# Performance work log

Measured on AMD Instinct MI355X. Metric: run time of the kernel, lower is better.

Reference implementation:

```python
import jax, jax.numpy as jnp
import numpy as np

N = 96                       # max_num_nodes == input_dim
LATENT = 256
OUT_DIM = N * (N + 1) // 2   # 4656
MPM_ITERS = 50


def setup_inputs() -> dict:
    key = jax.random.key(0)
    ks = jax.random.split(key, 8)
    s = 0.05
    return {
        "input_features": jax.random.normal(ks[0], (1, N, N), jnp.float32),
        "adj": jax.random.uniform(ks[1], (1, N, N), jnp.float32),
        "eps": jax.random.normal(ks[2], (1, LATENT), jnp.float32),
        "We11": jax.random.normal(ks[3], (N * N, LATENT), jnp.float32) * s,
        "be11": jnp.zeros((LATENT,), jnp.float32),
        "We12": jax.random.normal(ks[4], (N * N, LATENT), jnp.float32) * s,
        "be12": jnp.zeros((LATENT,), jnp.float32),
        "Wd1": jax.random.normal(ks[5], (LATENT, LATENT), jnp.float32) * s,
        "bd1": jnp.zeros((LATENT,), jnp.float32),
        "Wd2": jax.random.normal(ks[6], (LATENT, OUT_DIM), jnp.float32) * s,
        "bd2": jnp.zeros((OUT_DIM,), jnp.float32),
    }


def _bce(inp, tgt):
    # torch F.binary_cross_entropy(input=inp, target=tgt) with log clamp -100
    li = jnp.clip(jnp.log(inp), -100.0)
    l1 = jnp.clip(jnp.log1p(-inp), -100.0)
    return -jnp.mean(tgt * li + (1.0 - tgt) * l1)


def reference(input_features, adj, eps, We11, be11, We12, be12, Wd1, bd1, Wd2, bd2):
    # ---- MLP_VAE_plain ----
    h = input_features.reshape(-1, N * N)              # [1, N*N]
    z_mu = h @ We11 + be11
    z_ls = h @ We12 + be12
    z = eps * jnp.exp(0.5 * z_ls) + z_mu
    y = jax.nn.relu(z @ Wd1 + bd1) @ Wd2 + bd2         # [1, OUT_DIM]
    out = jax.nn.sigmoid(y)

    # ---- recover recon adjacency from triu vector (detached in original) ----
    iu, ju = jnp.triu_indices(N)
    up = jnp.zeros((N, N), jnp.float32).at[iu, ju].set(out[0])
    adj_rec = up + up.T - jnp.diag(jnp.diag(up))

    adj0 = adj[0]
    feat = jnp.sum(adj0, axis=1)                       # degree features
    feat_r = jnp.sum(adj_rec, axis=1)

    # ---- edge similarity tensor S[i,j,a,b] (vectorized O(N^4)) ----
    d = jnp.diag(adj0)
    dr = jnp.diag(adj_rec)
    A = adj0 * d[:, None] * d[None, :]                 # adj[i,j]*adj[i,i]*adj[j,j]
    B = adj_rec * dr[:, None] * dr[None, :]
    off = 1.0 - jnp.eye(N, dtype=jnp.float32)
    S = (A * off)[:, :, None, None] * (B * off)[None, None, :, :]  # i!=j, a!=b
    sim = 1.0 / (jnp.abs(feat[:, None] - feat_r[None, :]) + 1.0)   # deg_feature_similarity
    Sd = d[:, None] * dr[None, :] * sim                # S[i,i,a,a]
    r = jnp.arange(N)
    S = S.at[r[:, None], r[:, None], r[None, :], r[None, :]].set(Sd)

    # ---- max-pool matching (mpm), 50 iterations ----
    x0 = jnp.full((N, N), 1.0 / N, jnp.float32)

    def step(x, _):
        pooled = jnp.max(S * x[None, :, None, :], axis=3)          # [i,j,a]
        x_new = x * Sd + jnp.einsum('ija,ij->ia', pooled, off)     # sum over j != i
        return x_new / jnp.linalg.norm(x_new), None

    assignment, _ = jax.lax.scan(step, x0, None, length=MPM_ITERS)
    # (original then calls scipy Hungarian and only prints; result is unused in loss)

    # ---- loss ----
    adj_vec = adj0[iu, ju]                             # detached in original
    recon_loss = _bce(adj_vec, out[0])
    kl = -0.5 * jnp.sum(1.0 + z_ls - z_mu ** 2 - jnp.exp(z_ls)) / (N * N)
    loss = recon_loss + kl
    return loss, assignment
```

## Files before the change

kernel.cpp:

```cpp
#include <hip/hip_runtime.h>
#include <math.h>

typedef unsigned long long ull;

#define N      96
#define NN     9216
#define LAT    256
#define ODIM   4656
#define CH     128
#define RPC    72
#define ITERS  50
#define CB     12
#define CT     768
#define CPB    8

#define SGNMASK2 0x8000000080000000ULL
#define ABSMASK2 0x7FFFFFFF7FFFFFFFULL

#define WS_PART  0
#define WS_OUTS  65536
#define WS_KL    70192
#define WS_BCE   70193
#define WS_NSLOT 70208
#define WS_XBUF  70592

__device__ __forceinline__ int tri(int i, int j) {
    return i * N - i * (i - 1) / 2 + (j - i);
}

__device__ __forceinline__ int tri_row(int o) {
    int i = (int)floorf((193.0f - sqrtf((float)(37249 - 8 * o))) * 0.5f);
    i = max(0, min(95, i));
    while ((i + 1) * N - (i + 1) * i / 2 <= o) ++i;
    while (i * N - i * (i - 1) / 2 > o) --i;
    return i;
}

__global__ __launch_bounds__(256) void kA_gemv(const float* __restrict__ h,
                                               const float* __restrict__ W1,
                                               const float* __restrict__ W2,
                                               float* __restrict__ ws) {
    __shared__ float hs[RPC];
    int t = threadIdx.x, c = blockIdx.x;
    if (c == 0) {
        if (t < 2) ws[WS_KL + t] = 0.f;
        if (t < CB * 16) {
            ws[WS_NSLOT + t]           = 0.0f;
            ws[WS_NSLOT + CB * 16 + t] = -0.0f;
        }
    }
    for (int z = c * 256 + t; z < NN; z += CH * 256) {
        ws[WS_XBUF + z]      = 0.0f;
        ws[WS_XBUF + NN + z] = -0.0f;
    }
    int k0 = c * RPC;
    if (t < RPC) hs[t] = h[k0 + t];
    __syncthreads();
    float a1 = 0.f, a2 = 0.f;
    #pragma unroll 4
    for (int kk = 0; kk < RPC; ++kk) {
        float hv = hs[kk];
        a1 = fmaf(hv, W1[(k0 + kk) * LAT + t], a1);
        a2 = fmaf(hv, W2[(k0 + kk) * LAT + t], a2);
    }
    ws[WS_PART + c * LAT + t]        = a1;
    ws[WS_PART + (CH + c) * LAT + t] = a2;
}

__global__ __launch_bounds__(256) void kB_dec(const float* __restrict__ eps,
                                              const float* __restrict__ be11,
                                              const float* __restrict__ be12,
                                              const float* __restrict__ Wd1,
                                              const float* __restrict__ bd1,
                                              const float* __restrict__ Wd2,
                                              const float* __restrict__ bd2,
                                              const float* __restrict__ adj,
                                              float* __restrict__ ws) {
    __shared__ float zi[LAT];
    __shared__ float hid[LAT];
    __shared__ float red[256];
    int t = threadIdx.x;
    const float* p = ws + WS_PART;
    float mu = 0.f, ls = 0.f;
    #pragma unroll 8
    for (int c = 0; c < CH; ++c) {
        mu += p[c * LAT + t];
        ls += p[(CH + c) * LAT + t];
    }
    mu += be11[t];
    ls += be12[t];
    zi[t] = eps[t] * expf(0.5f * ls) + mu;
    red[t] = 1.0f + ls - mu * mu - expf(ls);
    __syncthreads();
    for (int s = 128; s > 0; s >>= 1) {
        if (t < s) red[t] += red[t + s];
        __syncthreads();
    }
    if (blockIdx.x == 0 && t == 0) ws[WS_KL] = -0.5f * red[0] / 9216.0f;
    __syncthreads();
    float acc = 0.f;
    #pragma unroll 8
    for (int k = 0; k < LAT; ++k) acc = fmaf(zi[k], Wd1[k * LAT + t], acc);
    hid[t] = fmaxf(acc + bd1[t], 0.f);
    __syncthreads();
    int o = blockIdx.x * 256 + t;
    float term = 0.f;
    if (o < ODIM) {
        float a2 = 0.f;
        #pragma unroll 8
        for (int k = 0; k < LAT; ++k) a2 = fmaf(hid[k], Wd2[k * ODIM + o], a2);
        float y = a2 + bd2[o];
        float s = 1.0f / (1.0f + expf(-y));
        ws[WS_OUTS + o] = s;
        int i = tri_row(o);
        int j = i + (o - (i * N - i * (i - 1) / 2));
        float inp = adj[i * N + j];
        float li = fmaxf(logf(inp), -100.0f);
        float l1 = fmaxf(log1pf(-inp), -100.0f);
        term = s * li + (1.0f - s) * l1;
    }
    red[t] = term;
    __syncthreads();
    for (int s = 128; s > 0; s >>= 1) {
        if (t < s) red[t] += red[t + s];
        __syncthreads();
    }
    if (t == 0) atomicAdd(ws + WS_BCE, red[0]);
}

__global__ __launch_bounds__(CT, 3) void kC_mpm(const float* __restrict__ adj,
                                                float* __restrict__ ws,
                                                float* __restrict__ out) {
    __shared__ __align__(16) float xn[N][100];
    __shared__ __align__(16) float Brow[CPB][N];
    __shared__ __align__(16) float Scol[CPB][N];
    __shared__ __align__(16) float Mv[CPB][N];
    __shared__ __align__(16) float Pout[N][CPB];
    __shared__ float ds[N], drs[N], ft[N];
    __shared__ float ftr_sh[CPB];
    __shared__ float wred[CT / 64];
    __shared__ float s_inv;

    int t = threadIdx.x, bid = blockIdx.x;
    int jj = t % N, al = t / N;
    int a  = bid * CPB + al;
    int si = t >> 3, sc = t & 7;

    const float* outs = ws + WS_OUTS;
    float* xbuf  = ws + WS_XBUF;
    float* nslot = ws + WS_NSLOT;

    if (t < N) {
        ds[t]  = adj[t * N + t];
        drs[t] = outs[tri(t, t)];
        const float4* ar = (const float4*)(adj + t * N);
        float s1 = 0.f;
        #pragma unroll
        for (int q = 0; q < N / 4; ++q) {
            float4 v = ar[q];
            s1 += v.x + v.y + v.z + v.w;
        }
        ft[t] = s1;
    }
    __syncthreads();
    {
        int lo = min(a, jj), hi = max(a, jj);
        Mv[al][jj] = outs[tri(lo, hi)];
    }
    __syncthreads();
    if (t < CPB) {
        float s2 = 0.f;
        for (int b = 0; b < N; ++b) s2 += Mv[t][b];
        ftr_sh[t] = s2;
    }
    __syncthreads();
    Brow[al][jj] = (jj == a) ? 0.f : (Mv[al][jj] * drs[a]) * drs[jj];
    Scol[al][jj] = (ds[jj] * drs[a]) * (1.0f / (fabsf(ft[jj] - ftr_sh[al]) + 1.0f));

    float arow[N];
    {
        const float* arp = adj + jj * N;
        float di = ds[jj];
        #pragma unroll
        for (int j = 0; j < N; ++j)
            arow[j] = (j == jj) ? 0.f : (arp[j] * di) * ds[j];
    }
    __syncthreads();

    float acc = 0.f;
    for (int s = 0; s < ITERS; ++s) {
        if (s == 0) {
            const float v0 = (float)(1.0 / 96.0);
            for (int f = t; f < NN; f += CT) xn[f / N][f % N] = v0;
            if (t == 0) s_inv = 1.0f;
        } else {
            const ull want = ((s >> 1) & 1) ? SGNMASK2 : 0ULL;
            const ull* src = (const ull*)(xbuf + (s & 1) * NN) + (si * 48 + sc * 6);
            union { ull u[6]; float4 q[3]; } U;
            bool ok = false;
            while (!ok) {
                ok = true;
                #pragma unroll
                for (int k = 0; k < 6; ++k)
                    U.u[k] = __hip_atomic_load(&src[k], __ATOMIC_RELAXED,
                                               __HIP_MEMORY_SCOPE_AGENT);
                #pragma unroll
                for (int k = 0; k < 6; ++k)
                    ok &= ((U.u[k] & SGNMASK2) == want);
                if (!ok) __builtin_amdgcn_s_sleep(1);
            }
            #pragma unroll
            for (int k = 0; k < 6; ++k) U.u[k] &= ABSMASK2;
            float4* dst = (float4*)&xn[si][sc * 12];
            dst[0] = U.q[0]; dst[1] = U.q[1]; dst[2] = U.q[2];
        }
        __syncthreads();

        float m = 0.f;
        #pragma unroll
        for (int q = 0; q < N / 4; ++q) {
            float4 xv = *(const float4*)&xn[jj][q * 4];
            float4 bw = *(const float4*)&Brow[al][q * 4];
            m = fmaxf(m, bw.x * xv.x);
            m = fmaxf(m, bw.y * xv.y);
            m = fmaxf(m, bw.z * xv.z);
            m = fmaxf(m, bw.w * xv.w);
        }
        Mv[al][jj] = m;

        if (s > 0 && t < 64) {
            const unsigned esn = (unsigned)((s >> 1) & 1);
            float pv = 0.f;
            bool done = (t >= CB);
            const unsigned* np = (const unsigned*)(nslot + (s & 1) * CB * 16);
            while (!__all(done)) {
                if (!done) {
                    unsigned u = __hip_atomic_load(&np[t * 16], __ATOMIC_RELAXED,
                                                   __HIP_MEMORY_SCOPE_AGENT);
                    if ((u >> 31) == esn) { pv = __uint_as_float(u & 0x7FFFFFFFu); done = true; }
                }
                __builtin_amdgcn_s_sleep(1);
            }
            #pragma unroll
            for (int off = 8; off > 0; off >>= 1) pv += __shfl_xor(pv, off, 16);
            if (t == 0) s_inv = 1.0f / sqrtf(pv);
        }
        __syncthreads();

        float r = xn[jj][a] * Scol[al][jj];
        #pragma unroll
        for (int q = 0; q < N / 4; ++q) {
            float4 mv = *(const float4*)&Mv[al][q * 4];
            r = fmaf(arow[q * 4 + 0], mv.x, r);
            r = fmaf(arow[q * 4 + 1], mv.y, r);
            r = fmaf(arow[q * 4 + 2], mv.z, r);
            r = fmaf(arow[q * 4 + 3], mv.w, r);
        }
        acc = r * s_inv;
        Pout[jj][al] = acc;

        float ssq = acc * acc;
        #pragma unroll
        for (int off = 32; off > 0; off >>= 1) ssq += __shfl_xor(ssq, off);
        if ((t & 63) == 0) wred[t >> 6] = ssq;
        __syncthreads();

        const unsigned tag1 = (unsigned)(((s + 1) >> 1) & 1);
        if (s < ITERS - 1 && t < 384) {
            int jjp = t >> 2, c = t & 3;
            float2 pr = *(const float2*)&Pout[jjp][c * 2];
            ull v = (ull)__float_as_uint(pr.x) | ((ull)__float_as_uint(pr.y) << 32);
            if (tag1) v |= SGNMASK2;
            __hip_atomic_store((ull*)(xbuf + ((s + 1) & 1) * NN) + (jjp * 48 + bid * 4 + c),
                               v, __ATOMIC_RELAXED, __HIP_MEMORY_SCOPE_AGENT);
        }
        if (t == 0) {
            float sum = 0.f;
            #pragma unroll
            for (int w = 0; w < CT / 64; ++w) sum += wred[w];
            unsigned u = __float_as_uint(sum) | (tag1 << 31);
            __hip_atomic_store((unsigned*)(nslot + ((s + 1) & 1) * CB * 16 + bid * 16),
                               u, __ATOMIC_RELAXED, __HIP_MEMORY_SCOPE_AGENT);
        }
    }

    if (t < 64) {
        const unsigned esf = (unsigned)((ITERS >> 1) & 1);
        float pv = 0.f;
        bool done = (t >= CB);
        const unsigned* np = (const unsigned*)(nslot + (ITERS & 1) * CB * 16);
        while (!__all(done)) {
            if (!done) {
                unsigned u = __hip_atomic_load(&np[t * 16], __ATOMIC_RELAXED,
                                               __HIP_MEMORY_SCOPE_AGENT);
                if ((u >> 31) == esf) { pv = __uint_as_float(u & 0x7FFFFFFFu); done = true; }
            }
            __builtin_amdgcn_s_sleep(1);
        }
        #pragma unroll
        for (int off = 8; off > 0; off >>= 1) pv += __shfl_xor(pv, off, 16);
        if (t == 0) s_inv = 1.0f / sqrtf(pv);
    }
    __syncthreads();
    out[1 + jj * N + a] = acc * s_inv;
    if (bid == 0 && t == 0)
        out[0] = -(ws[WS_BCE] / 4656.0f) + ws[WS_KL];
}

extern "C" void kernel_launch(void* const* d_in, const int* in_sizes, int n_in,
                              void* d_out, int out_size, void* d_ws, size_t ws_size,
                              hipStream_t stream) {
    const float* inf  = (const float*)d_in[0];
    const float* adj  = (const float*)d_in[1];
    const float* eps  = (const float*)d_in[2];
    const float* We11 = (const float*)d_in[3];
    const float* be11 = (const float*)d_in[4];
    const float* We12 = (const float*)d_in[5];
    const float* be12 = (const float*)d_in[6];
    const float* Wd1  = (const float*)d_in[7];
    const float* bd1  = (const float*)d_in[8];
    const float* Wd2  = (const float*)d_in[9];
    const float* bd2  = (const float*)d_in[10];
    float* ws  = (float*)d_ws;
    float* out = (float*)d_out;

    kA_gemv<<<CH, 256, 0, stream>>>(inf, We11, We12, ws);
    kB_dec <<<19, 256, 0, stream>>>(eps, be11, be12, Wd1, bd1, Wd2, bd2, adj, ws);
    kC_mpm <<<CB, CT, 0, stream>>>(adj, ws, out);
}
```

Before: 426.9 us.

## Read remote x slices directly from global per thread, dropping shared x staging

```diff
diff --git a/kernel.cpp b/kernel.cpp
--- a/kernel.cpp
+++ b/kernel.cpp
@@ -131,7 +131,6 @@
 __global__ __launch_bounds__(CT, 3) void kC_mpm(const float* __restrict__ adj,
                                                 float* __restrict__ ws,
                                                 float* __restrict__ out) {
-    __shared__ __align__(16) float xn[N][100];
     __shared__ __align__(16) float Brow[CPB][N];
     __shared__ __align__(16) float Scol[CPB][N];
     __shared__ __align__(16) float Mv[CPB][N];
@@ -144,7 +143,6 @@
     int t = threadIdx.x, bid = blockIdx.x;
     int jj = t % N, al = t / N;
     int a  = bid * CPB + al;
-    int si = t >> 3, sc = t & 7;
 
     const float* outs = ws + WS_OUTS;
     float* xbuf  = ws + WS_XBUF;
@@ -189,42 +187,55 @@
 
     float acc = 0.f;
     for (int s = 0; s < ITERS; ++s) {
+        float m = 0.f;
+        float xown;
         if (s == 0) {
             const float v0 = (float)(1.0 / 96.0);
-            for (int f = t; f < NN; f += CT) xn[f / N][f % N] = v0;
+            xown = v0;
+            #pragma unroll
+            for (int q = 0; q < N / 4; ++q) {
+                float4 bw = *(const float4*)&Brow[al][q * 4];
+                m = fmaxf(m, fmaxf(fmaxf(bw.x, bw.y), fmaxf(bw.z, bw.w)));
+            }
+            m *= v0;
             if (t == 0) s_inv = 1.0f;
         } else {
-            const ull want = ((s >> 1) & 1) ? SGNMASK2 : 0ULL;
-            const ull* src = (const ull*)(xbuf + (s & 1) * NN) + (si * 48 + sc * 6);
-            union { ull u[6]; float4 q[3]; } U;
-            bool ok = false;
-            while (!ok) {
-                ok = true;
+            xown = Pout[jj][al];
+            {
+                const float* bq = &Brow[al][bid * CPB];
                 #pragma unroll
-                for (int k = 0; k < 6; ++k)
-                    U.u[k] = __hip_atomic_load(&src[k], __ATOMIC_RELAXED,
-                                               __HIP_MEMORY_SCOPE_AGENT);
-                #pragma unroll
-                for (int k = 0; k < 6; ++k)
-                    ok &= ((U.u[k] & SGNMASK2) == want);
-                if (!ok) __builtin_amdgcn_s_sleep(1);
-            }
-            #pragma unroll
-            for (int k = 0; k < 6; ++k) U.u[k] &= ABSMASK2;
-            float4* dst = (float4*)&xn[si][sc * 12];
-            dst[0] = U.q[0]; dst[1] = U.q[1]; dst[2] = U.q[2];
-        }
-        __syncthreads();
-
-        float m = 0.f;
-        #pragma unroll
-        for (int q = 0; q < N / 4; ++q) {
-            float4 xv = *(const float4*)&xn[jj][q * 4];
-            float4 bw = *(const float4*)&Brow[al][q * 4];
-            m = fmaxf(m, bw.x * xv.x);
-            m = fmaxf(m, bw.y * xv.y);
-            m = fmaxf(m, bw.z * xv.z);
-            m = fmaxf(m, bw.w * xv.w);
+                for (int c = 0; c < CPB; ++c)
+                    m = fmaxf(m, bq[c] * Pout[jj][c]);
+            }
+            const ull want2 = ((s >> 1) & 1) ? SGNMASK2 : 0ULL;
+            const ull* bank = (const ull*)(xbuf + (s & 1) * NN);
+            #pragma unroll 1
+            for (int qi = 1; qi < CB; ++qi) {
+                int q = bid + qi; if (q >= CB) q -= CB;
+                const ull* p = bank + jj * 48 + q * 4;
+                ull v0, v1, v2, v3;
+                for (;;) {
+                    v0 = __hip_atomic_load(p + 0, __ATOMIC_RELAXED, __HIP_MEMORY_SCOPE_AGENT);
+                    v1 = __hip_atomic_load(p + 1, __ATOMIC_RELAXED, __HIP_MEMORY_SCOPE_AGENT);
+                    v2 = __hip_atomic_load(p + 2, __ATOMIC_RELAXED, __HIP_MEMORY_SCOPE_AGENT);
+                    v3 = __hip_atomic_load(p + 3, __ATOMIC_RELAXED, __HIP_MEMORY_SCOPE_AGENT);
+                    bool okk = ((v0 & SGNMASK2) == want2) & ((v1 & SGNMASK2) == want2) &
+                               ((v2 & SGNMASK2) == want2) & ((v3 & SGNMASK2) == want2);
+                    if (okk) break;
+                    __builtin_amdgcn_s_sleep(1);
+                }
+                v0 &= ABSMASK2; v1 &= ABSMASK2; v2 &= ABSMASK2; v3 &= ABSMASK2;
+                float4 bq0 = *(const float4*)&Brow[al][q * CPB];
+                float4 bq1 = *(const float4*)&Brow[al][q * CPB + 4];
+                m = fmaxf(m, bq0.x * __uint_as_float((unsigned)v0));
+                m = fmaxf(m, bq0.y * __uint_as_float((unsigned)(v0 >> 32)));
+                m = fmaxf(m, bq0.z * __uint_as_float((unsigned)v1));
+                m = fmaxf(m, bq0.w * __uint_as_float((unsigned)(v1 >> 32)));
+                m = fmaxf(m, bq1.x * __uint_as_float((unsigned)v2));
+                m = fmaxf(m, bq1.y * __uint_as_float((unsigned)(v2 >> 32)));
+                m = fmaxf(m, bq1.z * __uint_as_float((unsigned)v3));
+                m = fmaxf(m, bq1.w * __uint_as_float((unsigned)(v3 >> 32)));
+            }
         }
         Mv[al][jj] = m;
 
@@ -247,7 +258,7 @@
         }
         __syncthreads();
 
-        float r = xn[jj][a] * Scol[al][jj];
+        float r = xown * Scol[al][jj];
         #pragma unroll
         for (int q = 0; q < N / 4; ++q) {
             float4 mv = *(const float4*)&Mv[al][q * 4];
```

After: 1.276 ms. 2.99x slower.

## Transpose exchanged x buffer layout and publish results directly from registers

Applied to the files above, without the earlier changes.

```diff
diff --git a/kernel.cpp b/kernel.cpp
--- a/kernel.cpp
+++ b/kernel.cpp
@@ -131,11 +131,10 @@
 __global__ __launch_bounds__(CT, 3) void kC_mpm(const float* __restrict__ adj,
                                                 float* __restrict__ ws,
                                                 float* __restrict__ out) {
-    __shared__ __align__(16) float xn[N][100];
-    __shared__ __align__(16) float Brow[CPB][N];
-    __shared__ __align__(16) float Scol[CPB][N];
-    __shared__ __align__(16) float Mv[CPB][N];
-    __shared__ __align__(16) float Pout[N][CPB];
+    __shared__ float xnT[N][97];
+    __shared__ float Brow[CPB][N];
+    __shared__ float Scol[CPB][N];
+    __shared__ float Mv[CPB][N];
     __shared__ float ds[N], drs[N], ft[N];
     __shared__ float ftr_sh[CPB];
     __shared__ float wred[CT / 64];
@@ -144,7 +143,6 @@
     int t = threadIdx.x, bid = blockIdx.x;
     int jj = t % N, al = t / N;
     int a  = bid * CPB + al;
-    int si = t >> 3, sc = t & 7;
 
     const float* outs = ws + WS_OUTS;
     float* xbuf  = ws + WS_XBUF;
@@ -191,63 +189,64 @@
     for (int s = 0; s < ITERS; ++s) {
         if (s == 0) {
             const float v0 = (float)(1.0 / 96.0);
-            for (int f = t; f < NN; f += CT) xn[f / N][f % N] = v0;
+            for (int f = t; f < NN; f += CT) xnT[f / N][f % N] = v0;
             if (t == 0) s_inv = 1.0f;
         } else {
             const ull want = ((s >> 1) & 1) ? SGNMASK2 : 0ULL;
-            const ull* src = (const ull*)(xbuf + (s & 1) * NN) + (si * 48 + sc * 6);
-            union { ull u[6]; float4 q[3]; } U;
+            const ull* src = (const ull*)(xbuf + (s & 1) * NN);
+            ull v[6];
             bool ok = false;
             while (!ok) {
                 ok = true;
                 #pragma unroll
                 for (int k = 0; k < 6; ++k)
-                    U.u[k] = __hip_atomic_load(&src[k], __ATOMIC_RELAXED,
-                                               __HIP_MEMORY_SCOPE_AGENT);
+                    v[k] = __hip_atomic_load(&src[k * CT + t], __ATOMIC_RELAXED,
+                                             __HIP_MEMORY_SCOPE_AGENT);
                 #pragma unroll
                 for (int k = 0; k < 6; ++k)
-                    ok &= ((U.u[k] & SGNMASK2) == want);
+                    ok &= ((v[k] & SGNMASK2) == want);
                 if (!ok) __builtin_amdgcn_s_sleep(1);
             }
             #pragma unroll
-            for (int k = 0; k < 6; ++k) U.u[k] &= ABSMASK2;
-            float4* dst = (float4*)&xn[si][sc * 12];
-            dst[0] = U.q[0]; dst[1] = U.q[1]; dst[2] = U.q[2];
+            for (int k = 0; k < 6; ++k) {
+                ull w = v[k] & ABSMASK2;
+                int e = (k * CT + t) * 2;
+                int ac = e / N, i = e % N;
+                xnT[ac][i]     = __uint_as_float((unsigned)w);
+                xnT[ac][i + 1] = __uint_as_float((unsigned)(w >> 32));
+            }
+            if (t < 64) {
+                const unsigned esn = (unsigned)((s >> 1) & 1);
+                float pv = 0.f;
+                bool done = (t >= CB);
+                const unsigned* np = (const unsigned*)(nslot + (s & 1) * CB * 16);
+                while (!__all(done)) {
+                    if (!done) {
+                        unsigned u = __hip_atomic_load(&np[t * 16], __ATOMIC_RELAXED,
+                                                       __HIP_MEMORY_SCOPE_AGENT);
+                        if ((u >> 31) == esn) { pv = __uint_as_float(u & 0x7FFFFFFFu); done = true; }
+                    }
+                    __builtin_amdgcn_s_sleep(1);
+                }
+                #pragma unroll
+                for (int off = 8; off > 0; off >>= 1) pv += __shfl_xor(pv, off, 16);
+                if (t == 0) s_inv = 1.0f / sqrtf(pv);
+            }
         }
         __syncthreads();
 
         float m = 0.f;
         #pragma unroll
-        for (int q = 0; q < N / 4; ++q) {
-            float4 xv = *(const float4*)&xn[jj][q * 4];
-            float4 bw = *(const float4*)&Brow[al][q * 4];
-            m = fmaxf(m, bw.x * xv.x);
-            m = fmaxf(m, bw.y * xv.y);
-            m = fmaxf(m, bw.z * xv.z);
-            m = fmaxf(m, bw.w * xv.w);
+        for (int bq = 0; bq < N / 4; ++bq) {
+            m = fmaxf(m, Brow[al][bq * 4 + 0] * xnT[bq * 4 + 0][jj]);
+            m = fmaxf(m, Brow[al][bq * 4 + 1] * xnT[bq * 4 + 1][jj]);
+            m = fmaxf(m, Brow[al][bq * 4 + 2] * xnT[bq * 4 + 2][jj]);
+            m = fmaxf(m, Brow[al][bq * 4 + 3] * xnT[bq * 4 + 3][jj]);
         }
         Mv[al][jj] = m;
-
-        if (s > 0 && t < 64) {
-            const unsigned esn = (unsigned)((s >> 1) & 1);
-            float pv = 0.f;
-            bool done = (t >= CB);
-            const unsigned* np = (const unsigned*)(nslot + (s & 1) * CB * 16);
-            while (!__all(done)) {
-                if (!done) {
-                    unsigned u = __hip_atomic_load(&np[t * 16], __ATOMIC_RELAXED,
-                                                   __HIP_MEMORY_SCOPE_AGENT);
-                    if ((u >> 31) == esn) { pv = __uint_as_float(u & 0x7FFFFFFFu); done = true; }
-                }
-                __builtin_amdgcn_s_sleep(1);
-            }
-            #pragma unroll
-            for (int off = 8; off > 0; off >>= 1) pv += __shfl_xor(pv, off, 16);
-            if (t == 0) s_inv = 1.0f / sqrtf(pv);
-        }
-        __syncthreads();
-
-        float r = xn[jj][a] * Scol[al][jj];
+        __syncthreads();
+
+        float r = xnT[a][jj] * Scol[al][jj];
         #pragma unroll
         for (int q = 0; q < N / 4; ++q) {
             float4 mv = *(const float4*)&Mv[al][q * 4];
@@ -257,23 +256,21 @@
             r = fmaf(arow[q * 4 + 3], mv.w, r);
         }
         acc = r * s_inv;
-        Pout[jj][al] = acc;
+
+        const unsigned tag1 = (unsigned)(((s + 1) >> 1) & 1);
+        float nx = __shfl_down(acc, 1);
+        if (s < ITERS - 1 && (t & 1) == 0) {
+            ull pv = (ull)__float_as_uint(acc) | ((ull)__float_as_uint(nx) << 32);
+            if (tag1) pv |= SGNMASK2;
+            __hip_atomic_store((ull*)(xbuf + ((s + 1) & 1) * NN) + ((a * N + jj) >> 1),
+                               pv, __ATOMIC_RELAXED, __HIP_MEMORY_SCOPE_AGENT);
+        }
 
         float ssq = acc * acc;
         #pragma unroll
         for (int off = 32; off > 0; off >>= 1) ssq += __shfl_xor(ssq, off);
         if ((t & 63) == 0) wred[t >> 6] = ssq;
         __syncthreads();
-
-        const unsigned tag1 = (unsigned)(((s + 1) >> 1) & 1);
-        if (s < ITERS - 1 && t < 384) {
-            int jjp = t >> 2, c = t & 3;
-            float2 pr = *(const float2*)&Pout[jjp][c * 2];
-            ull v = (ull)__float_as_uint(pr.x) | ((ull)__float_as_uint(pr.y) << 32);
-            if (tag1) v |= SGNMASK2;
-            __hip_atomic_store((ull*)(xbuf + ((s + 1) & 1) * NN) + (jjp * 48 + bid * 4 + c),
-                               v, __ATOMIC_RELAXED, __HIP_MEMORY_SCOPE_AGENT);
-        }
         if (t == 0) {
             float sum = 0.f;
             #pragma unroll
```

After: 365.9 us. 14.3% less time.
